# Kernel optimization log

Hardware: AMD Instinct MI355X
Metric: run time of the kernel (lower is better)

The kernel has to match this reference:

```python
import jax, jax.numpy as jnp
import numpy as np

N = 50000   # nodes
E = 800000  # edges (avg degree 16)
C = 128     # hidden_channels
G = 128     # graphs in batch
L0, L1 = 512, 256  # linear_hidden_channels
P = 2       # num_params (output per graph)


def setup_inputs() -> dict:
    key = jax.random.key(0)
    ks = iter(jax.random.split(key, 48))

    def w(shape):
        return jax.random.normal(next(ks), shape, jnp.float32) / np.float32(np.sqrt(shape[0]))

    inp = {}
    inp["x"] = jax.random.normal(next(ks), (N, 4), jnp.float32)
    inp["edge_index"] = jax.random.randint(next(ks), (2, E), 0, N, dtype=jnp.int32)
    inp["edge_attr"] = jax.random.normal(next(ks), (E, 3), jnp.float32)
    inp["batch"] = jnp.sort(jax.random.randint(next(ks), (N,), 0, G, dtype=jnp.int32))
    # TransformerConv params: layer 0 (in=4) and shared layer (in=C, applied twice
    # because `[GConv(...)]*(n-1)` reuses the same module object).
    for i, din in enumerate([4, C]):
        inp[f"Wq{i}"] = w((din, C)); inp[f"bq{i}"] = jnp.zeros((C,), jnp.float32)
        inp[f"Wk{i}"] = w((din, C)); inp[f"bk{i}"] = jnp.zeros((C,), jnp.float32)
        inp[f"Wv{i}"] = w((din, C)); inp[f"bv{i}"] = jnp.zeros((C,), jnp.float32)
        inp[f"We{i}"] = w((3, C))   # lin_edge has no bias
        inp[f"Ws{i}"] = w((din, C)); inp[f"bs{i}"] = jnp.zeros((C,), jnp.float32)
    inp["Wl0"] = w((C, L0));  inp["bl0"] = jnp.zeros((L0,), jnp.float32)
    inp["Wl1"] = w((L0, L1)); inp["bl1"] = jnp.zeros((L1,), jnp.float32)
    inp["Wl2"] = w((L1, P));  inp["bl2"] = jnp.zeros((P,), jnp.float32)
    return inp


def tconv(x, src, dst, e_attr, Wq, bq, Wk, bk, Wv, bv, We, Ws, bs):
    # TransformerConv (heads=1, edge_dim, root_weight=True, beta=False)
    n = x.shape[0]
    c = Wq.shape[1]
    q = x @ Wq + bq            # [N, C]
    k = x @ Wk + bk
    v = x @ Wv + bv
    e = e_attr @ We            # [E, C]
    kj = k[src] + e            # [E, C] key at source + edge emb
    vj = v[src] + e            # [E, C] value at source + edge emb
    logits = jnp.sum(q[dst] * kj, axis=-1) / jnp.sqrt(jnp.float32(c))  # [E]
    # softmax over incoming edges of each target node
    m = jax.ops.segment_max(logits, dst, num_segments=n)
    a = jnp.exp(logits - m[dst])
    denom = jax.ops.segment_sum(a, dst, num_segments=n)
    alpha = a / denom[dst]
    out = jax.ops.segment_sum(vj * alpha[:, None], dst, num_segments=n)
    return out + x @ Ws + bs   # root/skip connection


def reference(x, edge_index, edge_attr, batch,
              Wq0, bq0, Wk0, bk0, Wv0, bv0, We0, Ws0, bs0,
              Wq1, bq1, Wk1, bk1, Wv1, bv1, We1, Ws1, bs1,
              Wl0, bl0, Wl1, bl1, Wl2, bl2):
    src, dst = edge_index[0], edge_index[1]
    # layer 0
    h = tconv(x, src, dst, edge_attr, Wq0, bq0, Wk0, bk0, Wv0, bv0, We0, Ws0, bs0)
    h = jax.nn.leaky_relu(h, 0.01)  # dropout is identity in eval
    # layers 1..2 share weights (Python list-multiplication of modules)
    for _ in range(2):
        h = tconv(h, src, dst, edge_attr, Wq1, bq1, Wk1, bk1, Wv1, bv1, We1, Ws1, bs1)
        h = jax.nn.leaky_relu(h, 0.01)
    # global_add_pool
    g = jax.ops.segment_sum(h, batch, num_segments=G)  # [G, C]
    # MLP head
    g = jax.nn.relu(g @ Wl0 + bl0)
    g = jax.nn.relu(g @ Wl1 + bl1)
    g = g @ Wl2 + bl2                                  # [G, 2]
    return jnp.ravel(g)                                # [G*2]
```

## Files before the change

### kernel.cpp

```cpp
#include <hip/hip_runtime.h>
#include <math.h>

#define N_NODES 50000
#define N_EDGES 800000
#define CDIM    128
#define GDIM    128
#define L0DIM   512
#define L1DIM   256

typedef unsigned int uint;
typedef unsigned short ushort;
typedef __attribute__((ext_vector_type(8))) short short8;
typedef __attribute__((ext_vector_type(4))) float f32x4;

__device__ inline ushort f2bf(float f) {
  uint u = __float_as_uint(f);
  uint r = (u + 0x7fffu + ((u >> 16) & 1u)) >> 16;
  return (ushort)r;
}
__device__ inline float bflo(uint u) { return __uint_as_float(u << 16); }
__device__ inline float bfhi(uint u) { return __uint_as_float(u & 0xffff0000u); }

__global__ void hist_kernel(const int* __restrict__ dst, int* counts, int E) {
  int e = blockIdx.x * 256 + threadIdx.x;
  if (e < E) atomicAdd(&counts[dst[e]], 1);
}

__global__ void scan_blocks(const int* __restrict__ counts, int* excl, int* bsums, int N) {
  __shared__ int s[1024];
  int tid = threadIdx.x;
  int i = blockIdx.x * 1024 + tid;
  int v = (i < N) ? counts[i] : 0;
  s[tid] = v;
  __syncthreads();
  for (int off = 1; off < 1024; off <<= 1) {
    int t = (tid >= off) ? s[tid - off] : 0;
    __syncthreads();
    s[tid] += t;
    __syncthreads();
  }
  if (i < N) excl[i] = s[tid] - v;
  if (tid == 1023) bsums[blockIdx.x] = s[1023];
}

__global__ void scan_sums(int* bsums, int nb) {
  int lane = threadIdx.x;
  int orig = (lane < nb) ? bsums[lane] : 0;
  int v = orig;
#pragma unroll
  for (int off = 1; off < 64; off <<= 1) {
    int t = __shfl_up(v, off);
    if (lane >= off) v += t;
  }
  if (lane < nb) bsums[lane] = v - orig;
}

__global__ void scan_add(const int* __restrict__ excl, const int* __restrict__ bsums,
                         int* indptr, int N, int E) {
  int i = blockIdx.x * 1024 + threadIdx.x;
  if (i < N) indptr[i] = excl[i] + bsums[blockIdx.x];
  if (i == 0) indptr[N] = E;
}

__global__ void scatter2_kernel(const int* __restrict__ dst, const int* __restrict__ src,
                                const float* __restrict__ attr,
                                const int* __restrict__ indptr,
                                int* cursor, int* csr_src, float4* csr_attr, int E) {
  int e = blockIdx.x * 256 + threadIdx.x;
  if (e < E) {
    int d = dst[e];
    int pos = atomicAdd(&cursor[d], 1);
    int i = indptr[d] + pos;
    csr_src[i] = src[e];
    csr_attr[i] = make_float4(attr[e * 3 + 0], attr[e * 3 + 1], attr[e * 3 + 2], 0.f);
  }
}

__global__ void l0_qkvs(const float* __restrict__ x,
                        const float* __restrict__ Wq, const float* __restrict__ bq,
                        const float* __restrict__ Wk, const float* __restrict__ bk,
                        const float* __restrict__ Wv, const float* __restrict__ bv,
                        const float* __restrict__ Ws, const float* __restrict__ bs,
                        float* __restrict__ q, ushort* __restrict__ kvb,
                        float* __restrict__ hs, int N) {
  __shared__ float W[4][4][128];
  __shared__ float B[4][128];
  int tid = threadIdx.x;
  for (int i = tid; i < 4 * 128; i += 256) {
    W[0][i >> 7][i & 127] = Wq[i];
    W[1][i >> 7][i & 127] = Wk[i];
    W[2][i >> 7][i & 127] = Wv[i];
    W[3][i >> 7][i & 127] = Ws[i];
  }
  for (int i = tid; i < 128; i += 256) {
    B[0][i] = bq[i]; B[1][i] = bk[i]; B[2][i] = bv[i]; B[3][i] = bs[i];
  }
  __syncthreads();
  int gid = blockIdx.x * 256 + tid;
  int n = gid >> 7, c = gid & 127;
  if (n >= N) return;
  float x0 = x[n * 4 + 0], x1 = x[n * 4 + 1], x2 = x[n * 4 + 2], x3 = x[n * 4 + 3];
  float qv = x0 * W[0][0][c] + x1 * W[0][1][c] + x2 * W[0][2][c] + x3 * W[0][3][c] + B[0][c];
  float kv = x0 * W[1][0][c] + x1 * W[1][1][c] + x2 * W[1][2][c] + x3 * W[1][3][c] + B[1][c];
  float vv = x0 * W[2][0][c] + x1 * W[2][1][c] + x2 * W[2][2][c] + x3 * W[2][3][c] + B[2][c];
  float sv = x0 * W[3][0][c] + x1 * W[3][1][c] + x2 * W[3][2][c] + x3 * W[3][3][c] + B[3][c];
  q[n * 128 + c] = qv;
  kvb[(size_t)n * 256 + c]       = f2bf(kv);
  kvb[(size_t)n * 256 + 128 + c] = f2bf(vv);
  hs[n * 128 + c] = sv;
}

__global__ void prep_w(const float* __restrict__ Wq, const float* __restrict__ Wk,
                       const float* __restrict__ Wv, const float* __restrict__ Ws,
                       ushort* __restrict__ wt) {
  int idx = blockIdx.x * 256 + threadIdx.x;
  int z = idx >> 14, rem = idx & 16383;
  int k_ = rem >> 7, c_ = rem & 127;
  const float* W = (z == 0) ? Wq : (z == 1) ? Wk : (z == 2) ? Wv : Ws;
  wt[z * 16384 + c_ * 128 + k_] = f2bf(W[k_ * 128 + c_]);
}

#define LDA 136
__global__ __launch_bounds__(256) void gemm_mfma(
    const float* __restrict__ H, const ushort* __restrict__ wtg,
    const float* __restrict__ bq, const float* __restrict__ bk,
    const float* __restrict__ bv, const float* __restrict__ bs,
    float* __restrict__ q, ushort* __restrict__ kvb,
    float* __restrict__ hs, int N) {
  int z = blockIdx.z;
  const float* bb = (z == 0) ? bq : (z == 1) ? bk : (z == 2) ? bv : bs;
  __shared__ ushort Alds[64 * LDA];
  __shared__ ushort Wlds[128 * LDA];
  int tid = threadIdx.x;
  int n0 = blockIdx.x * 64;

  {
    const uint* wg = (const uint*)(wtg + z * 16384);
    uint* wl = (uint*)Wlds;
    for (int i = tid; i < 8192; i += 256) {
      int c_ = i >> 6, kp = i & 63;
      wl[c_ * (LDA / 2) + kp] = wg[c_ * 64 + kp];
    }
  }
  {
    uint* al = (uint*)Alds;
    for (int i = tid; i < 4096; i += 256) {
      int r = i >> 6, kp = i & 63;
      int grow = n0 + r; grow = (grow < N) ? grow : (N - 1);
      float2 hv = *(const float2*)&H[(size_t)grow * 128 + 2 * kp];
      al[r * (LDA / 2) + kp] = (uint)f2bf(hv.x) | ((uint)f2bf(hv.y) << 16);
    }
  }
  __syncthreads();

  int w = tid >> 6, lane = tid & 63;
  int m_ = lane & 15, quad = lane >> 4;
  f32x4 acc[8];
#pragma unroll
  for (int ct = 0; ct < 8; ct++) acc[ct] = 0.f;

#pragma unroll
  for (int kc = 0; kc < 4; kc++) {
    short8 af = *(const short8*)&Alds[(w * 16 + m_) * LDA + kc * 32 + quad * 8];
#pragma unroll
    for (int ct = 0; ct < 8; ct++) {
      short8 bf = *(const short8*)&Wlds[(ct * 16 + m_) * LDA + kc * 32 + quad * 8];
      acc[ct] = __builtin_amdgcn_mfma_f32_16x16x32_bf16(af, bf, acc[ct], 0, 0, 0);
    }
  }

#pragma unroll
  for (int ct = 0; ct < 8; ct++) {
    int col = ct * 16 + m_;
    float bcol = bb[col];
#pragma unroll
    for (int reg = 0; reg < 4; reg++) {
      int n = n0 + w * 16 + quad * 4 + reg;
      if (n < N) {
        float o = acc[ct][reg] + bcol;
        if (z == 0)      q[(size_t)n * 128 + col] = o;
        else if (z == 3) hs[(size_t)n * 128 + col] = o;
        else             kvb[(size_t)n * 256 + ((z == 2) ? 128 : 0) + col] = f2bf(o);
      }
    }
  }
}

__global__ __launch_bounds__(256) void attn_fused(
    const float* __restrict__ q, const ushort* __restrict__ kv,
    const int* __restrict__ indptr, const int* __restrict__ csr_src,
    const float4* __restrict__ csr_attr, const float* __restrict__ We,
    float* __restrict__ h, int N) {
  __shared__ float WeS[384];
  int tid = threadIdx.x;
  for (int i = tid; i < 384; i += 256) WeS[i] = We[i];
  __syncthreads();
  int lane = tid & 63;
  int n = blockIdx.x * 4 + (tid >> 6);
  if (n >= N) return;
  int g = lane >> 4, gl = lane & 15;
  int c = gl * 8;
  float4 qa  = *(const float4*)&q[(size_t)n * 128 + c];
  float4 qb4 = *(const float4*)&q[(size_t)n * 128 + c + 4];
  float qv[8] = {qa.x, qa.y, qa.z, qa.w, qb4.x, qb4.y, qb4.z, qb4.w};
  float we0[8], we1[8], we2[8];
#pragma unroll
  for (int j = 0; j < 8; j++) {
    we0[j] = WeS[c + j]; we1[j] = WeS[128 + c + j]; we2[j] = WeS[256 + c + j];
  }
  float t0 = 0.f, t1 = 0.f, t2 = 0.f;
#pragma unroll
  for (int j = 0; j < 8; j++) {
    t0 = fmaf(we0[j], qv[j], t0);
    t1 = fmaf(we1[j], qv[j], t1);
    t2 = fmaf(we2[j], qv[j], t2);
  }
#pragma unroll
  for (int off = 1; off < 16; off <<= 1) {
    t0 += __shfl_xor(t0, off);
    t1 += __shfl_xor(t1, off);
    t2 += __shfl_xor(t2, off);
  }

  float4 sk0 = *(const float4*)&h[(size_t)n * 128 + c];
  float4 sk1 = *(const float4*)&h[(size_t)n * 128 + c + 4];
  int beg = indptr[n], end = indptr[n + 1];

  if (end > beg) {
    float m = -3.4e38f, d = 0.f;
    float sa0 = 0.f, sa1 = 0.f, sa2 = 0.f;
    float acc[8];
#pragma unroll
    for (int j = 0; j < 8; j++) acc[j] = 0.f;
    const uint* kvw = (const uint*)kv;
    int i = beg + g;
    int sj = 0; float4 at = make_float4(0.f, 0.f, 0.f, 0.f);
    if (i < end) { sj = csr_src[i]; at = csr_attr[i]; }
    for (; i < end; i += 4) {
      int sjc = sj; float4 atc = at;
      int inx = i + 4;
      if (inx < end) { sj = csr_src[inx]; at = csr_attr[inx]; }
      const uint4* kp = (const uint4*)(kvw + (size_t)sjc * 128);
      uint4 kr = kp[gl];
      uint4 vr = kp[16 + gl];
      float kx[8], vx[8];
      kx[0] = bflo(kr.x); kx[1] = bfhi(kr.x); kx[2] = bflo(kr.y); kx[3] = bfhi(kr.y);
      kx[4] = bflo(kr.z); kx[5] = bfhi(kr.z); kx[6] = bflo(kr.w); kx[7] = bfhi(kr.w);
      vx[0] = bflo(vr.x); vx[1] = bfhi(vr.x); vx[2] = bflo(vr.y); vx[3] = bfhi(vr.y);
      vx[4] = bflo(vr.z); vx[5] = bfhi(vr.z); vx[6] = bflo(vr.w); vx[7] = bfhi(vr.w);
      float p = 0.f;
#pragma unroll
      for (int j = 0; j < 8; j++) p = fmaf(qv[j], kx[j], p);
      p += __shfl_xor(p, 1); p += __shfl_xor(p, 2);
      p += __shfl_xor(p, 4); p += __shfl_xor(p, 8);
      p = fmaf(atc.x, t0, p);
      p = fmaf(atc.y, t1, p);
      p = fmaf(atc.z, t2, p);
      float l = p * 0.08838834764831845f;
      float nm = fmaxf(m, l);
      float sf = __expf(m - nm);
      float a = __expf(l - nm);
      d = d * sf + a;
      sa0 = sa0 * sf + a * atc.x;
      sa1 = sa1 * sf + a * atc.y;
      sa2 = sa2 * sf + a * atc.z;
#pragma unroll
      for (int j = 0; j < 8; j++) acc[j] = fmaf(acc[j], sf, a * vx[j]);
      m = nm;
    }
#pragma unroll
    for (int off = 16; off < 64; off <<= 1) {
      float m2 = __shfl_xor(m, off);
      float d2 = __shfl_xor(d, off);
      float nm = fmaxf(m, m2);
      float s1 = __expf(m - nm), s2 = __expf(m2 - nm);
      d = d * s1 + d2 * s2;
      sa0 = sa0 * s1 + __shfl_xor(sa0, off) * s2;
      sa1 = sa1 * s1 + __shfl_xor(sa1, off) * s2;
      sa2 = sa2 * s1 + __shfl_xor(sa2, off) * s2;
#pragma unroll
      for (int j = 0; j < 8; j++) {
        float a2 = __shfl_xor(acc[j], off);
        acc[j] = acc[j] * s1 + a2 * s2;
      }
      m = nm;
    }
    float inv = 1.f / d;
    float o[8];
#pragma unroll
    for (int j = 0; j < 8; j++) {
      float ecorr = sa0 * we0[j] + sa1 * we1[j] + sa2 * we2[j];
      o[j] = (acc[j] + ecorr) * inv;
    }
    sk0.x += o[0]; sk0.y += o[1]; sk0.z += o[2]; sk0.w += o[3];
    sk1.x += o[4]; sk1.y += o[5]; sk1.z += o[6]; sk1.w += o[7];
  }
  sk0.x = (sk0.x > 0.f) ? sk0.x : 0.01f * sk0.x;
  sk0.y = (sk0.y > 0.f) ? sk0.y : 0.01f * sk0.y;
  sk0.z = (sk0.z > 0.f) ? sk0.z : 0.01f * sk0.z;
  sk0.w = (sk0.w > 0.f) ? sk0.w : 0.01f * sk0.w;
  sk1.x = (sk1.x > 0.f) ? sk1.x : 0.01f * sk1.x;
  sk1.y = (sk1.y > 0.f) ? sk1.y : 0.01f * sk1.y;
  sk1.z = (sk1.z > 0.f) ? sk1.z : 0.01f * sk1.z;
  sk1.w = (sk1.w > 0.f) ? sk1.w : 0.01f * sk1.w;
  if (g == 0) {
    *(float4*)&h[(size_t)n * 128 + c] = sk0;
    *(float4*)&h[(size_t)n * 128 + c + 4] = sk1;
  }
}

__global__ void pool_kernel(const float* __restrict__ h, const int* __restrict__ batch,
                            float* __restrict__ gout, int N) {
  int tid = threadIdx.x;
  int sub = tid >> 6;
  int c = 2 * (tid & 63);
  int n0 = blockIdx.x * 64 + sub * 16;
  if (n0 >= N) return;
  int n1 = min(n0 + 16, N);
  float a0 = 0.f, a1 = 0.f;
  int cur = batch[n0];
  for (int n = n0; n < n1; n++) {
    int b = batch[n];
    if (b != cur) {
      atomicAdd(&gout[cur * 128 + c], a0);
      atomicAdd(&gout[cur * 128 + c + 1], a1);
      a0 = 0.f; a1 = 0.f; cur = b;
    }
    float2 hv = *(const float2*)&h[(size_t)n * 128 + c];
    a0 += hv.x; a1 += hv.y;
  }
  atomicAdd(&gout[cur * 128 + c], a0);
  atomicAdd(&gout[cur * 128 + c + 1], a1);
}

__global__ __launch_bounds__(256) void mlp_fused(
    const float* __restrict__ gp,
    const float* __restrict__ Wl0, const float* __restrict__ bl0,
    const float* __restrict__ Wl1, const float* __restrict__ bl1,
    const float* __restrict__ Wl2, const float* __restrict__ bl2,
    float* __restrict__ out) {
  int g = blockIdx.x;
  int tid = threadIdx.x;
  __shared__ float xin[CDIM];
  __shared__ float h1[L0DIM];
  __shared__ float h2[L1DIM];
  __shared__ float r0s[4], r1s[4];
  if (tid < CDIM) xin[tid] = gp[g * CDIM + tid];
  __syncthreads();
  for (int c = tid; c < L0DIM; c += 256) {
    float a0 = 0.f, a1 = 0.f, a2 = 0.f, a3 = 0.f;
#pragma unroll 4
    for (int kk = 0; kk < CDIM; kk += 4) {
      a0 = fmaf(xin[kk + 0], Wl0[(kk + 0) * L0DIM + c], a0);
      a1 = fmaf(xin[kk + 1], Wl0[(kk + 1) * L0DIM + c], a1);
      a2 = fmaf(xin[kk + 2], Wl0[(kk + 2) * L0DIM + c], a2);
      a3 = fmaf(xin[kk + 3], Wl0[(kk + 3) * L0DIM + c], a3);
    }
    h1[c] = fmaxf((a0 + a1) + (a2 + a3) + bl0[c], 0.f);
  }
  __syncthreads();
  {
    int c = tid;
    float a0 = 0.f, a1 = 0.f, a2 = 0.f, a3 = 0.f;
#pragma unroll 4
    for (int kk = 0; kk < L0DIM; kk += 4) {
      a0 = fmaf(h1[kk + 0], Wl1[(kk + 0) * L1DIM + c], a0);
      a1 = fmaf(h1[kk + 1], Wl1[(kk + 1) * L1DIM + c], a1);
      a2 = fmaf(h1[kk + 2], Wl1[(kk + 2) * L1DIM + c], a2);
      a3 = fmaf(h1[kk + 3], Wl1[(kk + 3) * L1DIM + c], a3);
    }
    h2[c] = fmaxf((a0 + a1) + (a2 + a3) + bl1[c], 0.f);
  }
  __syncthreads();
  float p0 = h2[tid] * Wl2[tid * 2 + 0];
  float p1 = h2[tid] * Wl2[tid * 2 + 1];
#pragma unroll
  for (int off = 32; off > 0; off >>= 1) {
    p0 += __shfl_down(p0, off);
    p1 += __shfl_down(p1, off);
  }
  int wv = tid >> 6, ln = tid & 63;
  if (ln == 0) { r0s[wv] = p0; r1s[wv] = p1; }
  __syncthreads();
  if (tid == 0) out[g * 2 + 0] = r0s[0] + r0s[1] + r0s[2] + r0s[3] + bl2[0];
  if (tid == 1) out[g * 2 + 1] = r1s[0] + r1s[1] + r1s[2] + r1s[3] + bl2[1];
}

extern "C" void kernel_launch(void* const* d_in, const int* in_sizes, int n_in,
                              void* d_out, int out_size, void* d_ws, size_t ws_size,
                              hipStream_t stream) {
  const int N = N_NODES, E = N_EDGES;
  const float* x    = (const float*)d_in[0];
  const int*   ei   = (const int*)d_in[1];
  const float* attr = (const float*)d_in[2];
  const int*   batch= (const int*)d_in[3];
  const int* src = ei;
  const int* dst = ei + E;

  const float *Wq0 = (const float*)d_in[4],  *bq0 = (const float*)d_in[5];
  const float *Wk0 = (const float*)d_in[6],  *bk0 = (const float*)d_in[7];
  const float *Wv0 = (const float*)d_in[8],  *bv0 = (const float*)d_in[9];
  const float *We0 = (const float*)d_in[10];
  const float *Ws0 = (const float*)d_in[11], *bs0 = (const float*)d_in[12];
  const float *Wq1 = (const float*)d_in[13], *bq1 = (const float*)d_in[14];
  const float *Wk1 = (const float*)d_in[15], *bk1 = (const float*)d_in[16];
  const float *Wv1 = (const float*)d_in[17], *bv1 = (const float*)d_in[18];
  const float *We1 = (const float*)d_in[19];
  const float *Ws1 = (const float*)d_in[20], *bs1 = (const float*)d_in[21];
  const float *Wl0 = (const float*)d_in[22], *bl0 = (const float*)d_in[23];
  const float *Wl1 = (const float*)d_in[24], *bl1 = (const float*)d_in[25];
  const float *Wl2 = (const float*)d_in[26], *bl2 = (const float*)d_in[27];

  size_t off = 0;
  auto carve = [&](size_t bytes) {
    void* p = (char*)d_ws + off;
    off += (bytes + 255) & ~(size_t)255;
    return p;
  };
  float*  hA       = (float*)carve((size_t)N * CDIM * 4);
  float*  hB       = (float*)carve((size_t)N * CDIM * 4);
  float*  qb       = (float*)carve((size_t)N * CDIM * 4);
  ushort* kvb      = (ushort*)carve((size_t)N * 256 * 2);
  int*    indptr   = (int*)carve((size_t)(N + 1) * 4);
  int*    csr_src  = (int*)carve((size_t)E * 4);
  float4* csr_attr = (float4*)carve((size_t)E * 16);
  int*    cc       = (int*)carve((size_t)2 * N * 4);
  int*    counts   = cc;
  int*    cursor   = cc + N;
  int*    excl     = (int*)carve((size_t)N * 4);
  int*    bsums    = (int*)carve((size_t)64 * 4);
  ushort* wt1      = (ushort*)carve((size_t)4 * 16384 * 2);
  float*  gp       = (float*)carve((size_t)GDIM * CDIM * 4);

  hipMemsetAsync(cc, 0, (size_t)2 * N * 4, stream);
  hipMemsetAsync(gp, 0, (size_t)GDIM * CDIM * 4, stream);

  int nscan = (N + 1023) / 1024;
  hist_kernel<<<(E + 255) / 256, 256, 0, stream>>>(dst, counts, E);
  scan_blocks<<<nscan, 1024, 0, stream>>>(counts, excl, bsums, N);
  scan_sums<<<1, 64, 0, stream>>>(bsums, nscan);
  scan_add<<<nscan, 1024, 0, stream>>>(excl, bsums, indptr, N, E);
  scatter2_kernel<<<(E + 255) / 256, 256, 0, stream>>>(dst, src, attr, indptr, cursor,
                                                       csr_src, csr_attr, E);
  prep_w<<<256, 256, 0, stream>>>(Wq1, Wk1, Wv1, Ws1, wt1);

  int naBlocks = (N + 3) / 4;
  dim3 gemmGrid((N + 63) / 64, 1, 4);

  l0_qkvs<<<(N * 128 + 255) / 256, 256, 0, stream>>>(
      x, Wq0, bq0, Wk0, bk0, Wv0, bv0, Ws0, bs0, qb, kvb, hA, N);
  attn_fused<<<naBlocks, 256, 0, stream>>>(qb, kvb, indptr, csr_src, csr_attr, We0, hA, N);

  gemm_mfma<<<gemmGrid, 256, 0, stream>>>(hA, wt1, bq1, bk1, bv1, bs1, qb, kvb, hB, N);
  attn_fused<<<naBlocks, 256, 0, stream>>>(qb, kvb, indptr, csr_src, csr_attr, We1, hB, N);

  gemm_mfma<<<gemmGrid, 256, 0, stream>>>(hB, wt1, bq1, bk1, bv1, bs1, qb, kvb, hA, N);
  attn_fused<<<naBlocks, 256, 0, stream>>>(qb, kvb, indptr, csr_src, csr_attr, We1, hA, N);

  pool_kernel<<<(N + 63) / 64, 256, 0, stream>>>(hA, batch, gp, N);
  mlp_fused<<<GDIM, 256, 0, stream>>>(gp, Wl0, bl0, Wl1, bl1, Wl2, bl2, (float*)d_out);
}
```

Before: 586.8 us.

## Prefetch next edge's K/V rows, use packed FMA and lazy softmax rescale

The edge loop in the fused attention kernel now issues the gathered K/V loads for the next edge one iteration ahead, hiding gather latency behind the current edge's math. The dot product and value accumulation use v_pk_fma_f32 on float pairs to halve the FMA instruction count. The online softmax only rescales accumulators when the logit exceeds the running max by more than 8, which skips one exp and many multiplies per edge. The trade-off is more live registers and slightly larger unnormalized intermediate values.

```diff
diff --git a/kernel.cpp b/kernel.cpp
--- a/kernel.cpp
+++ b/kernel.cpp
@@ -12,6 +12,7 @@
 typedef unsigned short ushort;
 typedef __attribute__((ext_vector_type(8))) short short8;
 typedef __attribute__((ext_vector_type(4))) float f32x4;
+typedef __attribute__((ext_vector_type(2))) float f32x2;
 
 __device__ inline ushort f2bf(float f) {
   uint u = __float_as_uint(f);
@@ -20,6 +21,18 @@
 }
 __device__ inline float bflo(uint u) { return __uint_as_float(u << 16); }
 __device__ inline float bfhi(uint u) { return __uint_as_float(u & 0xffff0000u); }
+
+__device__ inline f32x2 pkfma(f32x2 a, f32x2 b, f32x2 c) {
+  f32x2 d;
+  asm("v_pk_fma_f32 %0, %1, %2, %3" : "=v"(d) : "v"(a), "v"(b), "v"(c));
+  return d;
+}
+__device__ inline f32x2 bfpair(uint u) {
+  f32x2 r;
+  r.x = __uint_as_float(u << 16);
+  r.y = __uint_as_float(u & 0xffff0000u);
+  return r;
+}
 
 __global__ void hist_kernel(const int* __restrict__ dst, int* counts, int E) {
   int e = blockIdx.x * 256 + threadIdx.x;
@@ -202,7 +215,11 @@
   int c = gl * 8;
   float4 qa  = *(const float4*)&q[(size_t)n * 128 + c];
   float4 qb4 = *(const float4*)&q[(size_t)n * 128 + c + 4];
-  float qv[8] = {qa.x, qa.y, qa.z, qa.w, qb4.x, qb4.y, qb4.z, qb4.w};
+  f32x2 qv2[4];
+  qv2[0].x = qa.x;  qv2[0].y = qa.y;
+  qv2[1].x = qa.z;  qv2[1].y = qa.w;
+  qv2[2].x = qb4.x; qv2[2].y = qb4.y;
+  qv2[3].x = qb4.z; qv2[3].y = qb4.w;
   float we0[8], we1[8], we2[8];
 #pragma unroll
   for (int j = 0; j < 8; j++) {
@@ -210,10 +227,10 @@
   }
   float t0 = 0.f, t1 = 0.f, t2 = 0.f;
 #pragma unroll
-  for (int j = 0; j < 8; j++) {
-    t0 = fmaf(we0[j], qv[j], t0);
-    t1 = fmaf(we1[j], qv[j], t1);
-    t2 = fmaf(we2[j], qv[j], t2);
+  for (int j = 0; j < 4; j++) {
+    t0 = fmaf(we0[2*j], qv2[j].x, t0); t0 = fmaf(we0[2*j+1], qv2[j].y, t0);
+    t1 = fmaf(we1[2*j], qv2[j].x, t1); t1 = fmaf(we1[2*j+1], qv2[j].y, t1);
+    t2 = fmaf(we2[2*j], qv2[j].x, t2); t2 = fmaf(we2[2*j+1], qv2[j].y, t2);
   }
 #pragma unroll
   for (int off = 1; off < 16; off <<= 1) {
@@ -229,44 +246,65 @@
   if (end > beg) {
     float m = -3.4e38f, d = 0.f;
     float sa0 = 0.f, sa1 = 0.f, sa2 = 0.f;
-    float acc[8];
-#pragma unroll
-    for (int j = 0; j < 8; j++) acc[j] = 0.f;
+    f32x2 acc2[4];
+#pragma unroll
+    for (int j = 0; j < 4; j++) { acc2[j].x = 0.f; acc2[j].y = 0.f; }
     const uint* kvw = (const uint*)kv;
+
     int i = beg + g;
-    int sj = 0; float4 at = make_float4(0.f, 0.f, 0.f, 0.f);
-    if (i < end) { sj = csr_src[i]; at = csr_attr[i]; }
+    uint4 kr = make_uint4(0, 0, 0, 0), vr = make_uint4(0, 0, 0, 0);
+    float ax = 0.f, ay = 0.f, az = 0.f;
+    if (i < end) {
+      int sj = csr_src[i];
+      float4 at = csr_attr[i];
+      ax = at.x; ay = at.y; az = at.z;
+      const uint4* kp = (const uint4*)(kvw + (size_t)sj * 128);
+      kr = kp[gl]; vr = kp[16 + gl];
+    }
     for (; i < end; i += 4) {
-      int sjc = sj; float4 atc = at;
+      uint4 krc = kr, vrc = vr;
+      float axc = ax, ayc = ay, azc = az;
       int inx = i + 4;
-      if (inx < end) { sj = csr_src[inx]; at = csr_attr[inx]; }
-      const uint4* kp = (const uint4*)(kvw + (size_t)sjc * 128);
-      uint4 kr = kp[gl];
-      uint4 vr = kp[16 + gl];
-      float kx[8], vx[8];
-      kx[0] = bflo(kr.x); kx[1] = bfhi(kr.x); kx[2] = bflo(kr.y); kx[3] = bfhi(kr.y);
-      kx[4] = bflo(kr.z); kx[5] = bfhi(kr.z); kx[6] = bflo(kr.w); kx[7] = bfhi(kr.w);
-      vx[0] = bflo(vr.x); vx[1] = bfhi(vr.x); vx[2] = bflo(vr.y); vx[3] = bfhi(vr.y);
-      vx[4] = bflo(vr.z); vx[5] = bfhi(vr.z); vx[6] = bflo(vr.w); vx[7] = bfhi(vr.w);
-      float p = 0.f;
-#pragma unroll
-      for (int j = 0; j < 8; j++) p = fmaf(qv[j], kx[j], p);
+      if (inx < end) {
+        int sj = csr_src[inx];
+        float4 at = csr_attr[inx];
+        ax = at.x; ay = at.y; az = at.z;
+        const uint4* kp = (const uint4*)(kvw + (size_t)sj * 128);
+        kr = kp[gl]; vr = kp[16 + gl];
+      }
+      f32x2 k2[4], v2[4];
+      k2[0] = bfpair(krc.x); k2[1] = bfpair(krc.y);
+      k2[2] = bfpair(krc.z); k2[3] = bfpair(krc.w);
+      v2[0] = bfpair(vrc.x); v2[1] = bfpair(vrc.y);
+      v2[2] = bfpair(vrc.z); v2[3] = bfpair(vrc.w);
+      f32x2 p2a, p2b;
+      p2a.x = 0.f; p2a.y = 0.f; p2b.x = 0.f; p2b.y = 0.f;
+      p2a = pkfma(qv2[0], k2[0], p2a);
+      p2b = pkfma(qv2[1], k2[1], p2b);
+      p2a = pkfma(qv2[2], k2[2], p2a);
+      p2b = pkfma(qv2[3], k2[3], p2b);
+      float p = (p2a.x + p2a.y) + (p2b.x + p2b.y);
       p += __shfl_xor(p, 1); p += __shfl_xor(p, 2);
       p += __shfl_xor(p, 4); p += __shfl_xor(p, 8);
-      p = fmaf(atc.x, t0, p);
-      p = fmaf(atc.y, t1, p);
-      p = fmaf(atc.z, t2, p);
+      p = fmaf(axc, t0, p);
+      p = fmaf(ayc, t1, p);
+      p = fmaf(azc, t2, p);
       float l = p * 0.08838834764831845f;
-      float nm = fmaxf(m, l);
-      float sf = __expf(m - nm);
-      float a = __expf(l - nm);
-      d = d * sf + a;
-      sa0 = sa0 * sf + a * atc.x;
-      sa1 = sa1 * sf + a * atc.y;
-      sa2 = sa2 * sf + a * atc.z;
-#pragma unroll
-      for (int j = 0; j < 8; j++) acc[j] = fmaf(acc[j], sf, a * vx[j]);
-      m = nm;
+      if (l > m + 8.f) {
+        float sf = __expf(m - l);
+        d *= sf; sa0 *= sf; sa1 *= sf; sa2 *= sf;
+#pragma unroll
+        for (int j = 0; j < 4; j++) { acc2[j].x *= sf; acc2[j].y *= sf; }
+        m = l;
+      }
+      float a = __expf(l - m);
+      d += a;
+      sa0 = fmaf(a, axc, sa0);
+      sa1 = fmaf(a, ayc, sa1);
+      sa2 = fmaf(a, azc, sa2);
+      f32x2 a2; a2.x = a; a2.y = a;
+#pragma unroll
+      for (int j = 0; j < 4; j++) acc2[j] = pkfma(a2, v2[j], acc2[j]);
     }
 #pragma unroll
     for (int off = 16; off < 64; off <<= 1) {
@@ -279,18 +317,22 @@
       sa1 = sa1 * s1 + __shfl_xor(sa1, off) * s2;
       sa2 = sa2 * s1 + __shfl_xor(sa2, off) * s2;
 #pragma unroll
-      for (int j = 0; j < 8; j++) {
-        float a2 = __shfl_xor(acc[j], off);
-        acc[j] = acc[j] * s1 + a2 * s2;
+      for (int j = 0; j < 4; j++) {
+        float axm = __shfl_xor(acc2[j].x, off);
+        float aym = __shfl_xor(acc2[j].y, off);
+        acc2[j].x = acc2[j].x * s1 + axm * s2;
+        acc2[j].y = acc2[j].y * s1 + aym * s2;
       }
       m = nm;
     }
     float inv = 1.f / d;
     float o[8];
 #pragma unroll
-    for (int j = 0; j < 8; j++) {
-      float ecorr = sa0 * we0[j] + sa1 * we1[j] + sa2 * we2[j];
-      o[j] = (acc[j] + ecorr) * inv;
+    for (int j = 0; j < 4; j++) {
+      float e0 = sa0 * we0[2*j]   + sa1 * we1[2*j]   + sa2 * we2[2*j];
+      float e1 = sa0 * we0[2*j+1] + sa1 * we1[2*j+1] + sa2 * we2[2*j+1];
+      o[2*j]   = (acc2[j].x + e0) * inv;
+      o[2*j+1] = (acc2[j].y + e1) * inv;
     }
     sk0.x += o[0]; sk0.y += o[1]; sk0.z += o[2]; sk0.w += o[3];
     sk1.x += o[4]; sk1.y += o[5]; sk1.z += o[6]; sk1.w += o[7];
```

New measurement: 617.8 us. +5.3%, slower.
